# Kernel optimization log

Hardware: AMD Instinct MI355X
Metric: run time of the kernel (lower is better)

The kernel has to match this reference:

```python
import jax, jax.numpy as jnp
import numpy as np

N_NODES = 50000
N_EDGES = 800000
N_GRAPHS = 256
F_IN = 256
H_DIM = 64


def setup_inputs() -> dict:
    key = jax.random.key(0)
    ks = jax.random.split(key, 9)
    x = jax.random.normal(ks[0], (N_NODES, F_IN), dtype=jnp.float32)
    edge_index = jax.random.randint(ks[1], (2, N_EDGES), 0, N_NODES, dtype=jnp.int64)
    batch = jnp.sort(jax.random.randint(ks[2], (N_NODES,), 0, N_GRAPHS, dtype=jnp.int64))
    s = 1.0 / np.sqrt(F_IN)
    Wq = jax.random.normal(ks[3], (F_IN, H_DIM), dtype=jnp.float32) * s
    bq = jnp.zeros((H_DIM,), dtype=jnp.float32)
    Wk = jax.random.normal(ks[4], (F_IN, H_DIM), dtype=jnp.float32) * s
    bk = jnp.zeros((H_DIM,), dtype=jnp.float32)
    Wv = jax.random.normal(ks[5], (F_IN, H_DIM), dtype=jnp.float32) * s
    bv = jnp.zeros((H_DIM,), dtype=jnp.float32)
    return {"x": x, "Wq": Wq, "bq": bq, "Wk": Wk, "bk": bk, "Wv": Wv, "bv": bv,
            "edge_index": edge_index, "batch": batch}


def reference(x, Wq, bq, Wk, bk, Wv, bv, edge_index, batch):
    src, dest = edge_index[0], edge_index[1]
    # node projections then per-edge gathers
    q = (x @ Wq + bq)[dest]            # [E, h]
    k = (x @ Wk + bk)[src]             # [E, h]
    v = (x @ Wv + bv)[src]             # [E, h]
    # per-edge dot-product score (bmm of [E,1,h] x [E,h,1])
    prod = jnp.sum(k * q, axis=-1, keepdims=True) / np.sqrt(H_DIM)  # [E, 1]
    exp = jnp.exp(prod)
    seg = batch[src]                   # per-graph segment of source node
    denom = jax.ops.segment_sum(exp, seg, num_segments=N_GRAPHS)    # [G, 1]
    a = exp / (denom[seg] + 1e-6)      # [E, 1]
    out = jax.ops.segment_sum(v * a, dest, num_segments=N_NODES)    # [N, h]
    return out
```

## Files before the change

kernel.cpp:

```cpp
#include <hip/hip_runtime.h>

#define H    64
#define F    256
#define NSEG 256
#define SCB  2048
#define MB   64
#define KC   64
#define XPAD 72

typedef float          f32x4v __attribute__((ext_vector_type(4)));
typedef short          bf16x8 __attribute__((ext_vector_type(8)));
typedef unsigned short u16x4  __attribute__((ext_vector_type(4)));

__global__ __launch_bounds__(256) void hist_kernel(
    const int* __restrict__ ei, int* __restrict__ counts,
    int N, int E, int nspan)
{
    const int p  = blockIdx.x & 7;
    const int ci = blockIdx.x >> 3;
    const int lo = p * nspan;
    const int hi = min(N, lo + nspan);
    const int e0 = ci * 1024 + threadIdx.x * 4;
    if (e0 + 3 < E) {
        const int4 d4 = *(const int4*)(ei + E + e0);
        int d;
        d = min(max(d4.x, 0), N - 1); if (d >= lo && d < hi) atomicAdd(&counts[d], 1);
        d = min(max(d4.y, 0), N - 1); if (d >= lo && d < hi) atomicAdd(&counts[d], 1);
        d = min(max(d4.z, 0), N - 1); if (d >= lo && d < hi) atomicAdd(&counts[d], 1);
        d = min(max(d4.w, 0), N - 1); if (d >= lo && d < hi) atomicAdd(&counts[d], 1);
    } else {
        for (int e = e0; e < E; ++e) {
            int d = min(max(ei[E + e], 0), N - 1);
            if (d >= lo && d < hi) atomicAdd(&counts[d], 1);
        }
    }
}

#define CVT_WRITE(buf, rr, cc, val) do {                                      \
    const float ff_[4] = {(val).x, (val).y, (val).z, (val).w};                \
    u16x4 h_, l_;                                                             \
    _Pragma("unroll")                                                         \
    for (int u_ = 0; u_ < 4; ++u_) {                                          \
        unsigned ub_ = __float_as_uint(ff_[u_]);                              \
        h_[u_] = (unsigned short)(ub_ >> 16);                                 \
        float rf_ = ff_[u_] - __uint_as_float(ub_ & 0xFFFF0000u);             \
        l_[u_] = (unsigned short)(__float_as_uint(rf_) >> 16);                \
    }                                                                         \
    *(u16x4*)&xs_hi[buf][(rr) * XPAD + (cc) * 4] = h_;                        \
    *(u16x4*)&xs_lo[buf][(rr) * XPAD + (cc) * 4] = l_;                        \
} while (0)

__global__ __launch_bounds__(768, 3) void qkv_mfma(
    const float* __restrict__ x,
    const float* __restrict__ Wq, const float* __restrict__ Wk,
    const float* __restrict__ Wv,
    const float* __restrict__ bq, const float* __restrict__ bk,
    const float* __restrict__ bv,
    float* __restrict__ q, float* __restrict__ k, float* __restrict__ v,
    int N, int ntiles)
{
    __shared__ unsigned short xs_hi[2][MB * XPAD];
    __shared__ unsigned short xs_lo[2][MB * XPAD];

    const int t    = threadIdx.x;
    const int lane = t & 63;
    const int w    = t >> 6;
    const int mat  = w >> 2;
    const int ct   = w & 3;
    const int l15  = lane & 15;
    const int quad = lane >> 4;

    const float* Wm   = (mat == 0) ? Wq : (mat == 1) ? Wk : Wv;
    const float* bias = (mat == 0) ? bq : (mat == 1) ? bk : bv;
    float*       dst  = (mat == 0) ? q  : (mat == 1) ? k  : v;
    const int col = ct * 16 + l15;
    const float bb = bias[col];

    bf16x8 Bh[8], Bl[8];
    #pragma unroll
    for (int u = 0; u < 8; ++u) {
        #pragma unroll
        for (int j = 0; j < 8; ++j) {
            const float f = Wm[(size_t)(u * 32 + quad * 8 + j) * H + col];
            const unsigned ub = __float_as_uint(f);
            Bh[u][j] = (short)(ub >> 16);
            const float rf = f - __uint_as_float(ub & 0xFFFF0000u);
            Bl[u][j] = (short)(__float_as_uint(rf) >> 16);
        }
    }

    const int r0 = t >> 4;
    const int c0 = t & 15;
    const int r1 = (t + 768) >> 4;

    #pragma unroll 1
    for (int tile = blockIdx.x; tile < ntiles; tile += gridDim.x) {
        const int block0 = tile * MB;

        f32x4v acc[4];
        #pragma unroll
        for (int i = 0; i < 4; ++i) acc[i] = (f32x4v)0.f;

        float4 pv0, pv1;
        pv0 = *(const float4*)(x + (size_t)min(block0 + r0, N - 1) * F + c0 * 4);
        if (t < 256)
            pv1 = *(const float4*)(x + (size_t)min(block0 + r1, N - 1) * F + c0 * 4);
        CVT_WRITE(0, r0, c0, pv0);
        if (t < 256) CVT_WRITE(0, r1, c0, pv1);

        #pragma unroll
        for (int c = 0; c < 4; ++c) {
            __syncthreads();

            if (c < 3) {
                const int kb = (c + 1) * KC;
                pv0 = *(const float4*)(x + (size_t)min(block0 + r0, N - 1) * F + kb + c0 * 4);
                if (t < 256)
                    pv1 = *(const float4*)(x + (size_t)min(block0 + r1, N - 1) * F + kb + c0 * 4);
            }

            #pragma unroll
            for (int sk = 0; sk < 2; ++sk) {
                const int u = c * 2 + sk;
                #pragma unroll
                for (int mt = 0; mt < 4; ++mt) {
                    const int ao = (mt * 16 + l15) * XPAD + sk * 32 + quad * 8;
                    const bf16x8 ah = *(const bf16x8*)&xs_hi[c & 1][ao];
                    const bf16x8 al = *(const bf16x8*)&xs_lo[c & 1][ao];
                    f32x4v a = acc[mt];
                    a = __builtin_amdgcn_mfma_f32_16x16x32_bf16(ah, Bh[u], a, 0, 0, 0);
                    a = __builtin_amdgcn_mfma_f32_16x16x32_bf16(ah, Bl[u], a, 0, 0, 0);
                    a = __builtin_amdgcn_mfma_f32_16x16x32_bf16(al, Bh[u], a, 0, 0, 0);
                    acc[mt] = a;
                }
            }

            if (c < 3) {
                const int nb = (c & 1) ^ 1;
                CVT_WRITE(nb, r0, c0, pv0);
                if (t < 256) CVT_WRITE(nb, r1, c0, pv1);
            }
        }

        #pragma unroll
        for (int mt = 0; mt < 4; ++mt) {
            #pragma unroll
            for (int r = 0; r < 4; ++r) {
                const int node = block0 + mt * 16 + quad * 4 + r;
                if (node < N)
                    dst[(size_t)node * H + col] = acc[mt][r] + bb;
            }
        }
    }
}

__global__ __launch_bounds__(256) void scanA(
    const int* __restrict__ counts, int* __restrict__ offsets,
    int* __restrict__ bsum, int n)
{
    __shared__ int ps[256];
    const int t = threadIdx.x;
    const int i0 = blockIdx.x * SCB + t * 8;
    int loc[8];
    int s = 0;
    #pragma unroll
    for (int u = 0; u < 8; ++u) {
        int i = i0 + u;
        int c = (i < n) ? ((counts[i] + 3) & ~3) : 0;
        loc[u] = s; s += c;
    }
    ps[t] = s;
    __syncthreads();
    for (int off = 1; off < 256; off <<= 1) {
        int a = (t >= off) ? ps[t - off] : 0;
        __syncthreads();
        ps[t] += a;
        __syncthreads();
    }
    const int base = ps[t] - s;
    #pragma unroll
    for (int u = 0; u < 8; ++u) {
        int i = i0 + u;
        if (i < n) offsets[i] = base + loc[u];
    }
    if (t == 255) bsum[blockIdx.x] = ps[255];
}

__global__ void scanB(int* __restrict__ bsum, int nb)
{
    const int t = threadIdx.x;
    int v = (t < nb) ? bsum[t] : 0;
    int inc = v;
    #pragma unroll
    for (int off = 1; off < 64; off <<= 1) {
        int u = __shfl_up(inc, off, 64);
        if (t >= off) inc += u;
    }
    if (t < nb) bsum[t] = inc - v;
}

__global__ __launch_bounds__(256) void scanC(
    const int* __restrict__ bsum, int* __restrict__ offsets,
    int* __restrict__ cursor, int n)
{
    const int i0 = blockIdx.x * SCB + threadIdx.x * 8;
    const int add = bsum[blockIdx.x];
    #pragma unroll
    for (int u = 0; u < 8; ++u) {
        int i = i0 + u;
        if (i < n) { int o = offsets[i] + add; offsets[i] = o; cursor[i] = o; }
    }
}

__global__ __launch_bounds__(256) void reorder_kernel(
    const int* __restrict__ ei, const int* __restrict__ batch,
    int* __restrict__ cursor, unsigned* __restrict__ epack,
    int E, int N, int nspan)
{
    const int p  = blockIdx.x & 7;
    const int ci = blockIdx.x >> 3;
    const int lo = p * nspan;
    const int hi = min(N, lo + nspan);
    const int e0 = ci * 1024 + threadIdx.x * 4;

    int d[4];
    if (e0 + 3 < E) {
        const int4 d4 = *(const int4*)(ei + E + e0);
        d[0] = d4.x; d[1] = d4.y; d[2] = d4.z; d[3] = d4.w;
    } else {
        #pragma unroll
        for (int u = 0; u < 4; ++u)
            d[u] = (e0 + u < E) ? ei[E + e0 + u] : -1;
    }

    #pragma unroll
    for (int u = 0; u < 4; ++u) {
        const int dst = min(max(d[u], 0), N - 1);
        if (d[u] >= 0 && dst >= lo && dst < hi) {
            int src = ei[e0 + u];
            src = min(max(src, 0), N - 1);
            int seg = batch[src];
            seg = min(max(seg, 0), NSEG - 1);
            const int pos = atomicAdd(&cursor[dst], 1);
            epack[pos] = (unsigned)src | ((unsigned)seg << 16);
        }
    }
}

__global__ __launch_bounds__(256) void score_kernel(
    const float* __restrict__ q, const float* __restrict__ k,
    const unsigned* __restrict__ epack,
    const int* __restrict__ offsets, const int* __restrict__ counts,
    float* __restrict__ exps, float* __restrict__ denom8, int N)
{
    __shared__ float sden[NSEG];
    const int t = threadIdx.x;
    sden[t] = 0.f;
    __syncthreads();

    const int lane16 = t & 15;
    const int grp    = (t >> 4) & 3;
    const int wave   = t >> 6;
    const int nwaves = gridDim.x * 4;

    const float4* q4 = (const float4*)q;
    const float4* k4 = (const float4*)k;

    for (int n = blockIdx.x * 4 + wave; n < N; n += nwaves) {
        const int off = offsets[n];
        const int cnt = counts[n];
        if (cnt == 0) continue;
        const float4 qv = q4[(size_t)n * 16 + lane16];
        for (int i = grp; i < cnt; i += 4) {
            const int pos = off + i;
            const unsigned p = epack[pos];
            const int src = p & 0xFFFF;
            const float4 kv = k4[(size_t)src * 16 + lane16];
            float d = kv.x * qv.x + kv.y * qv.y + kv.z * qv.z + kv.w * qv.w;
            d += __shfl_xor(d, 1, 64);
            d += __shfl_xor(d, 2, 64);
            d += __shfl_xor(d, 4, 64);
            d += __shfl_xor(d, 8, 64);
            if (lane16 == 0) {
                float ex = __expf(d * 0.125f);
                exps[pos] = ex;
                atomicAdd(&sden[(p >> 16) & 255], ex);
            }
        }
    }
    __syncthreads();
    float ds = sden[t];
    if (ds != 0.f) atomicAdd(&denom8[(blockIdx.x & 7) * NSEG + t], ds);
}

__global__ __launch_bounds__(256) void accum_kernel(
    const float* __restrict__ v, const float* __restrict__ exps,
    const unsigned* __restrict__ epack,
    const int* __restrict__ offsets, const int* __restrict__ counts,
    const float* __restrict__ denom8, float* __restrict__ out, int N)
{
    __shared__ float rden[NSEG];
    const int t = threadIdx.x;
    {
        float dsum = 0.f;
        #pragma unroll
        for (int p = 0; p < 8; ++p) dsum += denom8[p * NSEG + t];
        rden[t] = 1.0f / (dsum + 1e-6f);
    }
    __syncthreads();

    const int lane = t & 63;
    const int wave = t >> 6;
    const int n = blockIdx.x * 4 + wave;
    if (n >= N) return;

    const int off = offsets[n];
    const int cnt = counts[n];

    float acc = 0.f;
    int i = 0;
    for (; i + 8 <= cnt; i += 8) {
        const uint4  pa = *(const uint4*)(epack + off + i);
        const uint4  pb = *(const uint4*)(epack + off + i + 4);
        const float4 ea = *(const float4*)(exps + off + i);
        const float4 eb = *(const float4*)(exps + off + i + 4);
        const float v0 = v[(size_t)(pa.x & 0xFFFF) * H + lane];
        const float v1 = v[(size_t)(pa.y & 0xFFFF) * H + lane];
        const float v2 = v[(size_t)(pa.z & 0xFFFF) * H + lane];
        const float v3 = v[(size_t)(pa.w & 0xFFFF) * H + lane];
        const float v4_ = v[(size_t)(pb.x & 0xFFFF) * H + lane];
        const float v5 = v[(size_t)(pb.y & 0xFFFF) * H + lane];
        const float v6 = v[(size_t)(pb.z & 0xFFFF) * H + lane];
        const float v7 = v[(size_t)(pb.w & 0xFFFF) * H + lane];
        acc = fmaf(v0, ea.x * rden[(pa.x >> 16) & 255], acc);
        acc = fmaf(v1, ea.y * rden[(pa.y >> 16) & 255], acc);
        acc = fmaf(v2, ea.z * rden[(pa.z >> 16) & 255], acc);
        acc = fmaf(v3, ea.w * rden[(pa.w >> 16) & 255], acc);
        acc = fmaf(v4_, eb.x * rden[(pb.x >> 16) & 255], acc);
        acc = fmaf(v5, eb.y * rden[(pb.y >> 16) & 255], acc);
        acc = fmaf(v6, eb.z * rden[(pb.z >> 16) & 255], acc);
        acc = fmaf(v7, eb.w * rden[(pb.w >> 16) & 255], acc);
    }
    for (; i + 4 <= cnt; i += 4) {
        const uint4  pp = *(const uint4*)(epack + off + i);
        const float4 ee = *(const float4*)(exps + off + i);
        const float v0 = v[(size_t)(pp.x & 0xFFFF) * H + lane];
        const float v1 = v[(size_t)(pp.y & 0xFFFF) * H + lane];
        const float v2 = v[(size_t)(pp.z & 0xFFFF) * H + lane];
        const float v3 = v[(size_t)(pp.w & 0xFFFF) * H + lane];
        acc = fmaf(v0, ee.x * rden[(pp.x >> 16) & 255], acc);
        acc = fmaf(v1, ee.y * rden[(pp.y >> 16) & 255], acc);
        acc = fmaf(v2, ee.z * rden[(pp.z >> 16) & 255], acc);
        acc = fmaf(v3, ee.w * rden[(pp.w >> 16) & 255], acc);
    }
    for (; i < cnt; ++i) {
        const unsigned p = epack[off + i];
        acc = fmaf(v[(size_t)(p & 0xFFFF) * H + lane],
                   exps[off + i] * rden[(p >> 16) & 255], acc);
    }
    out[(size_t)n * H + lane] = acc;
}

extern "C" void kernel_launch(void* const* d_in, const int* in_sizes, int n_in,
                              void* d_out, int out_size, void* d_ws, size_t ws_size,
                              hipStream_t stream)
{
    const float* x   = (const float*)d_in[0];
    const float* Wq  = (const float*)d_in[1];
    const float* bq  = (const float*)d_in[2];
    const float* Wk  = (const float*)d_in[3];
    const float* bk  = (const float*)d_in[4];
    const float* Wv  = (const float*)d_in[5];
    const float* bv  = (const float*)d_in[6];
    const int* ei    = (const int*)d_in[7];
    const int* batch = (const int*)d_in[8];

    const int N = in_sizes[8];
    const int E = in_sizes[7] / 2;
    const int EP = E + 3 * N + 16;

    float*    q       = (float*)d_ws;
    float*    k       = q + (size_t)N * H;
    float*    v       = k + (size_t)N * H;
    float*    exps    = v + (size_t)N * H;
    unsigned* epack   = (unsigned*)(exps + EP);
    int*      counts  = (int*)(epack + EP);
    int*      offsets = counts + N;
    int*      cursor  = offsets + N;
    int*      bsum    = cursor + N;
    float*    denom8  = (float*)(bsum + 64);

    hipMemsetAsync(counts, 0, N * sizeof(int), stream);
    hipMemsetAsync(denom8, 0, 8 * NSEG * sizeof(float), stream);

    const int NT    = (N + MB - 1) / MB;
    const int NC    = (E + 1023) / 1024;
    const int nspan = (N + 7) / 8;
    const int NBSC  = (N + SCB - 1) / SCB;

    hist_kernel<<<8 * NC, 256, 0, stream>>>(ei, counts, N, E, nspan);

    qkv_mfma<<<256, 768, 0, stream>>>(
        x, Wq, Wk, Wv, bq, bk, bv, q, k, v, N, NT);

    scanA<<<NBSC, 256, 0, stream>>>(counts, offsets, bsum, N);
    scanB<<<1, 64, 0, stream>>>(bsum, NBSC);
    scanC<<<NBSC, 256, 0, stream>>>(bsum, offsets, cursor, N);

    reorder_kernel<<<8 * NC, 256, 0, stream>>>(
        ei, batch, cursor, epack, E, N, nspan);

    score_kernel<<<2048, 256, 0, stream>>>(
        q, k, epack, offsets, counts, exps, denom8, N);

    accum_kernel<<<(N + 3) / 4, 256, 0, stream>>>(
        v, exps, epack, offsets, counts, denom8, (float*)d_out, N);
}
```

Measured before the change: 285.4 us.

## Build destination histogram in LDS per span and chunk, reduce partials in scan

Measured after the change: 267.9 us. -6.1%, faster.

```diff
diff --git a/kernel.cpp b/kernel.cpp
--- a/kernel.cpp
+++ b/kernel.cpp
@@ -7,33 +7,53 @@
 #define MB   64
 #define KC   64
 #define XPAD 72
+#define NSPAN_MAX 8192
 
 typedef float          f32x4v __attribute__((ext_vector_type(4)));
 typedef short          bf16x8 __attribute__((ext_vector_type(8)));
 typedef unsigned short u16x4  __attribute__((ext_vector_type(4)));
 
-__global__ __launch_bounds__(256) void hist_kernel(
-    const int* __restrict__ ei, int* __restrict__ counts,
+__global__ __launch_bounds__(1024) void hist8_kernel(
+    const int* __restrict__ ei, int* __restrict__ counts8,
     int N, int E, int nspan)
 {
+    __shared__ int lh[NSPAN_MAX];
     const int p  = blockIdx.x & 7;
-    const int ci = blockIdx.x >> 3;
+    const int c  = blockIdx.x >> 3;
     const int lo = p * nspan;
-    const int hi = min(N, lo + nspan);
-    const int e0 = ci * 1024 + threadIdx.x * 4;
-    if (e0 + 3 < E) {
-        const int4 d4 = *(const int4*)(ei + E + e0);
-        int d;
-        d = min(max(d4.x, 0), N - 1); if (d >= lo && d < hi) atomicAdd(&counts[d], 1);
-        d = min(max(d4.y, 0), N - 1); if (d >= lo && d < hi) atomicAdd(&counts[d], 1);
-        d = min(max(d4.z, 0), N - 1); if (d >= lo && d < hi) atomicAdd(&counts[d], 1);
-        d = min(max(d4.w, 0), N - 1); if (d >= lo && d < hi) atomicAdd(&counts[d], 1);
+    const int span = min(N - lo, nspan);
+    const int t = threadIdx.x;
+
+    for (int i = t; i < span; i += 1024) lh[i] = 0;
+    __syncthreads();
+
+    const int epc = (E + 7) >> 3;
+    const int e0 = c * epc;
+    const int e1 = min(E, e0 + epc);
+
+    if (((E + e0) & 3) == 0) {
+        const int nv = (e1 - e0) >> 2;
+        for (int i = t; i < nv; i += 1024) {
+            const int4 d4 = *(const int4*)(ei + E + e0 + i * 4);
+            int d;
+            d = min(max(d4.x, 0), N - 1) - lo; if ((unsigned)d < (unsigned)span) atomicAdd(&lh[d], 1);
+            d = min(max(d4.y, 0), N - 1) - lo; if ((unsigned)d < (unsigned)span) atomicAdd(&lh[d], 1);
+            d = min(max(d4.z, 0), N - 1) - lo; if ((unsigned)d < (unsigned)span) atomicAdd(&lh[d], 1);
+            d = min(max(d4.w, 0), N - 1) - lo; if ((unsigned)d < (unsigned)span) atomicAdd(&lh[d], 1);
+        }
+        for (int e = e0 + nv * 4 + t; e < e1; e += 1024) {
+            const int d = min(max(ei[E + e], 0), N - 1) - lo;
+            if ((unsigned)d < (unsigned)span) atomicAdd(&lh[d], 1);
+        }
     } else {
-        for (int e = e0; e < E; ++e) {
-            int d = min(max(ei[E + e], 0), N - 1);
-            if (d >= lo && d < hi) atomicAdd(&counts[d], 1);
-        }
-    }
+        for (int e = e0 + t; e < e1; e += 1024) {
+            const int d = min(max(ei[E + e], 0), N - 1) - lo;
+            if ((unsigned)d < (unsigned)span) atomicAdd(&lh[d], 1);
+        }
+    }
+    __syncthreads();
+
+    for (int i = t; i < span; i += 1024) counts8[(size_t)c * N + lo + i] = lh[i];
 }
 
 #define CVT_WRITE(buf, rr, cc, val) do {                                      \
@@ -155,8 +175,8 @@
 }
 
 __global__ __launch_bounds__(256) void scanA(
-    const int* __restrict__ counts, int* __restrict__ offsets,
-    int* __restrict__ bsum, int n)
+    const int* __restrict__ counts8, int* __restrict__ counts,
+    int* __restrict__ offsets, int* __restrict__ bsum, int n)
 {
     __shared__ int ps[256];
     const int t = threadIdx.x;
@@ -166,7 +186,13 @@
     #pragma unroll
     for (int u = 0; u < 8; ++u) {
         int i = i0 + u;
-        int c = (i < n) ? ((counts[i] + 3) & ~3) : 0;
+        int c = 0;
+        if (i < n) {
+            #pragma unroll
+            for (int p = 0; p < 8; ++p) c += counts8[(size_t)p * n + i];
+            counts[i] = c;
+            c = (c + 3) & ~3;
+        }
         loc[u] = s; s += c;
     }
     ps[t] = s;
@@ -389,8 +415,8 @@
     int*      cursor  = offsets + N;
     int*      bsum    = cursor + N;
     float*    denom8  = (float*)(bsum + 64);
-
-    hipMemsetAsync(counts, 0, N * sizeof(int), stream);
+    int*      counts8 = (int*)(denom8 + 8 * NSEG);
+
     hipMemsetAsync(denom8, 0, 8 * NSEG * sizeof(float), stream);
 
     const int NT    = (N + MB - 1) / MB;
@@ -398,12 +424,12 @@
     const int nspan = (N + 7) / 8;
     const int NBSC  = (N + SCB - 1) / SCB;
 
-    hist_kernel<<<8 * NC, 256, 0, stream>>>(ei, counts, N, E, nspan);
+    hist8_kernel<<<64, 1024, 0, stream>>>(ei, counts8, N, E, nspan);
 
     qkv_mfma<<<256, 768, 0, stream>>>(
         x, Wq, Wk, Wv, bq, bk, bv, q, k, v, N, NT);
 
-    scanA<<<NBSC, 256, 0, stream>>>(counts, offsets, bsum, N);
+    scanA<<<NBSC, 256, 0, stream>>>(counts8, counts, offsets, bsum, N);
     scanB<<<1, 64, 0, stream>>>(bsum, NBSC);
     scanC<<<NBSC, 256, 0, stream>>>(bsum, offsets, cursor, N);
 
```
